# Kernel optimization log

Hardware: AMD Instinct MI355X
Metric: run time of the kernel (lower is better)

The kernel has to match this reference:

```python
import jax, jax.numpy as jnp
import numpy as np

B, N, D = 256, 1024, 128
SCALING_FACTOR = 1.0


def setup_inputs() -> dict:
    key = jax.random.key(0)
    ks = jax.random.split(key, 7)
    d = jax.random.normal(ks[0], (B, N, D), dtype=jnp.float32)
    si = jax.random.normal(ks[1], (B, N, D), dtype=jnp.float32)
    sj = jax.random.normal(ks[2], (B, N, D), dtype=jnp.float32)
    mi = jax.random.randint(ks[3], (B, N), 0, 2).astype(bool)
    mj = jax.random.randint(ks[4], (B, N), 0, 2).astype(bool)
    # AvgModel.layer: Linear(D, D**2)
    W1 = jax.random.normal(ks[5], (D, D * D), dtype=jnp.float32) * 0.02
    b1 = jnp.zeros((D * D,), dtype=jnp.float32)
    # CondNNWAvgPRModel.layer: Linear(H=2D, 1)
    W2 = jax.random.normal(ks[6], (2 * D, 1), dtype=jnp.float32) * 0.02
    b2 = jnp.zeros((1,), dtype=jnp.float32)
    return {"d": d, "si": si, "sj": sj, "mi": mi, "mj": mj,
            "W1": W1, "b1": b1, "W2": W2, "b2": b2}


def reference(d, si, sj, mi, mj, W1, b1, W2, b2):
    # generate_transformation: M = relu(Linear(d[:,0,:])).reshape(B, D, D)
    dm = d[:, 0, :]                                   # [B, D]
    M = jax.nn.relu(dm @ W1 + b1).reshape(-1, D, D)    # [B, D, D]

    def predict(s, mask):
        # transform = bmm(x, M)
        td = jnp.einsum('bnd,bde->bne', d, M)          # [B, N, D]
        ts = jnp.einsum('bnd,bde->bne', s, M)          # [B, N, D]
        x = jnp.concatenate([td, ts], axis=2)          # [B, N, 2D]
        z = (x @ W2 + b2)[..., 0]                      # [B, N]
        # fused masked segment-sum replacing the Python loop
        return jnp.sum(z * mask.astype(z.dtype), axis=1)  # [B]

    score1 = predict(si, mi)
    score2 = predict(sj, mj)
    return jax.nn.sigmoid(SCALING_FACTOR * (score1 - score2))
```

## Files before the change

### kernel.cpp

```cpp
#include <hip/hip_runtime.h>
#include <math.h>

#define BB 256
#define NN 1024
#define DD 128
#define NCHUNK 4
#define ROWS (NN / NCHUNK)

#define PA_OFF   0
#define PCI_OFF  (NCHUNK*BB*DD)
#define PCJ_OFF  (2*NCHUNK*BB*DD)
#define PCNT_OFF (3*NCHUNK*BB*DD)
#define U_OFF    (PCNT_OFF + NCHUNK*BB)
#define V_OFF    (U_OFF + BB*DD)

typedef _Float16 f16x8 __attribute__((ext_vector_type(8)));
typedef float    f32x4 __attribute__((ext_vector_type(4)));

__global__ __launch_bounds__(256) void k1_sparse(
    const float* __restrict__ d, const float* __restrict__ si,
    const float* __restrict__ sj, const void* __restrict__ miv,
    const void* __restrict__ mjv, float* __restrict__ ws)
{
    const int chunk = blockIdx.x;
    const int b     = blockIdx.y;
    const int role  = blockIdx.z;
    const int t     = threadIdx.x;
    const int lane  = t & 31;
    const int rg    = t >> 5;
    const int wid   = t >> 6;
    const int l64   = t & 63;

    __shared__ int s_mode;
    if (t == 0) s_mode = 0;
    __syncthreads();
    {
        const unsigned int* a = (const unsigned int*)miv;
        const unsigned int* c = (const unsigned int*)mjv;
        if ((a[t] | c[t]) > 1u) s_mode = 1;
    }
    __syncthreads();
    const bool bytes_mode = (s_mode != 0);

    __shared__ float s_wc[ROWS];
    __shared__ short s_idx[ROWS];
    __shared__ int   s_wcnt[4];
    __shared__ int   s_woff[5];
    __shared__ int   s_cnt4[4];

    const int    n0      = chunk * ROWS;
    const size_t rowbase = (size_t)b * NN;

    float w;
    {
        const size_t m = rowbase + (size_t)(n0 + t);
        float fi, fj;
        if (bytes_mode) {
            fi = (float)((const unsigned char*)miv)[m];
            fj = (float)((const unsigned char*)mjv)[m];
        } else {
            fi = (float)((const int*)miv)[m];
            fj = (float)((const int*)mjv)[m];
        }
        w = (role == 0) ? (fi - fj) : ((role == 1) ? fi : fj);
        if (role == 0) {
            const unsigned long long bi = __ballot(fi != 0.f);
            const unsigned long long bj = __ballot(fj != 0.f);
            if (l64 == 0) s_cnt4[wid] = __popcll(bi) - __popcll(bj);
        }
    }
    const bool keep = (w != 0.f);
    const unsigned long long ball = __ballot(keep);
    const int prefix = __popcll(ball & ((1ull << l64) - 1ull));
    if (l64 == 0) s_wcnt[wid] = __popcll(ball);
    __syncthreads();
    if (t == 0) {
        int a0 = 0;
        #pragma unroll
        for (int ww = 0; ww < 4; ++ww) { s_woff[ww] = a0; a0 += s_wcnt[ww]; }
        s_woff[4] = a0;
        if (role == 0)
            ws[PCNT_OFF + chunk * BB + b] =
                (float)(s_cnt4[0] + s_cnt4[1] + s_cnt4[2] + s_cnt4[3]);
    }
    __syncthreads();
    const int K    = s_woff[4];
    const int Kpad = (K + 31) & ~31;
    if (keep) {
        const int pos = s_woff[wid] + prefix;
        s_idx[pos] = (short)t;
        s_wc[pos]  = w;
    }
    for (int p = K + t; p < Kpad; p += 256) { s_idx[p] = 0; s_wc[p] = 0.f; }
    __syncthreads();

    const float* src = (role == 0) ? d : ((role == 1) ? si : sj);
    const size_t cbase = (rowbase + (size_t)n0) * (size_t)DD
                       + (size_t)lane * 4;

    float acc[4] = {0.f, 0.f, 0.f, 0.f};

    for (int i = 0; i < Kpad; i += 32) {
        int   r[4];
        float wv[4];
        #pragma unroll
        for (int u = 0; u < 4; ++u) {
            const int p = i + u * 8 + rg;
            r[u]  = s_idx[p];
            wv[u] = s_wc[p];
        }
        float4 v[4];
        #pragma unroll
        for (int u = 0; u < 4; ++u)
            v[u] = *(const float4*)(src + cbase + (size_t)r[u] * DD);
        #pragma unroll
        for (int u = 0; u < 4; ++u) {
            acc[0] = fmaf(wv[u], v[u].x, acc[0]);
            acc[1] = fmaf(wv[u], v[u].y, acc[1]);
            acc[2] = fmaf(wv[u], v[u].z, acc[2]);
            acc[3] = fmaf(wv[u], v[u].w, acc[3]);
        }
    }

    __shared__ float red[256][5];
    #pragma unroll
    for (int i = 0; i < 4; ++i) red[t][i] = acc[i];
    __syncthreads();
    if (t < 128) {
        #pragma unroll
        for (int i = 0; i < 4; ++i) red[t][i] += red[t + 128][i];
    }
    __syncthreads();
    if (t < 64) {
        #pragma unroll
        for (int i = 0; i < 4; ++i) red[t][i] += red[t + 64][i];
    }
    __syncthreads();
    if (t < 32) {
        #pragma unroll
        for (int i = 0; i < 4; ++i) red[t][i] += red[t + 32][i];
        const size_t poff = ((role == 0) ? PA_OFF : ((role == 1) ? PCI_OFF
                                                                 : PCJ_OFF))
                          + ((size_t)chunk * BB + b) * DD;
        float* P = ws + poff;
        #pragma unroll
        for (int i = 0; i < 4; ++i) P[t * 4 + i] = red[t][i];
    }
}

__global__ __launch_bounds__(256) void k2_mfma(
    const float* __restrict__ d, const float* __restrict__ W1,
    const float* __restrict__ b1, const float* __restrict__ W2,
    float* __restrict__ ws)
{
    const int p    = blockIdx.x;
    const int b0   = blockIdx.y * 64;
    const int t    = threadIdx.x;
    const int wid  = t >> 6;
    const int lane = t & 63;
    const int lcol = lane & 15;
    const int lrow = lane >> 4;

    __shared__ _Float16 As[64][136];
    __shared__ _Float16 Bs[128][136];

    for (int idx = t; idx < 64 * 32; idx += 256) {
        const int bb = idx >> 5;
        const int k4 = (idx & 31) * 4;
        const float4 v = *(const float4*)(d + (size_t)(b0 + bb) * (NN * DD) + k4);
        As[bb][k4 + 0] = (_Float16)v.x;
        As[bb][k4 + 1] = (_Float16)v.y;
        As[bb][k4 + 2] = (_Float16)v.z;
        As[bb][k4 + 3] = (_Float16)v.w;
    }
    for (int idx = t; idx < 128 * 32; idx += 256) {
        const int k  = idx >> 5;
        const int c4 = (idx & 31) * 4;
        const float4 v =
            *(const float4*)(W1 + (size_t)k * 16384 + p * 128 + c4);
        Bs[c4 + 0][k] = (_Float16)v.x;
        Bs[c4 + 1][k] = (_Float16)v.y;
        Bs[c4 + 2][k] = (_Float16)v.z;
        Bs[c4 + 3][k] = (_Float16)v.w;
    }
    __syncthreads();

    f32x4 acc[8];
    #pragma unroll
    for (int n = 0; n < 8; ++n) acc[n] = (f32x4){0.f, 0.f, 0.f, 0.f};

    #pragma unroll
    for (int ks = 0; ks < 4; ++ks) {
        const int k0 = ks * 32;
        const f16x8 afrag = *(const f16x8*)&As[wid * 16 + lcol][k0 + lrow * 8];
        #pragma unroll
        for (int n = 0; n < 8; ++n) {
            const f16x8 bfrag =
                *(const f16x8*)&Bs[n * 16 + lcol][k0 + lrow * 8];
            acc[n] = __builtin_amdgcn_mfma_f32_16x16x32_f16(
                afrag, bfrag, acc[n], 0, 0, 0);
        }
    }

    float ua[4] = {0.f, 0.f, 0.f, 0.f};
    float va[4] = {0.f, 0.f, 0.f, 0.f};
    #pragma unroll
    for (int n = 0; n < 8; ++n) {
        const int c = n * 16 + lcol;
        const float bias = b1[p * 128 + c];
        const float w2a  = W2[c];
        const float w2b  = W2[128 + c];
        #pragma unroll
        for (int reg = 0; reg < 4; ++reg) {
            const float g = fmaxf(acc[n][reg] + bias, 0.f);
            ua[reg] = fmaf(g, w2a, ua[reg]);
            va[reg] = fmaf(g, w2b, va[reg]);
        }
    }
    #pragma unroll
    for (int off = 8; off > 0; off >>= 1) {
        #pragma unroll
        for (int reg = 0; reg < 4; ++reg) {
            ua[reg] += __shfl_xor(ua[reg], off, 64);
            va[reg] += __shfl_xor(va[reg], off, 64);
        }
    }
    if (lcol == 0) {
        #pragma unroll
        for (int reg = 0; reg < 4; ++reg) {
            const int b = b0 + wid * 16 + lrow * 4 + reg;
            ws[U_OFF + (size_t)b * DD + p] = ua[reg];
            ws[V_OFF + (size_t)b * DD + p] = va[reg];
        }
    }
}

__global__ __launch_bounds__(64) void k3_final(
    const float* __restrict__ ws, const float* __restrict__ b2p,
    float* __restrict__ out)
{
    const int b = blockIdx.x;
    const int l = threadIdx.x;

    float s = 0.f;
    #pragma unroll
    for (int rep = 0; rep < 2; ++rep) {
        const int k = l + rep * 64;
        float A = 0.f, Ci = 0.f, Cj = 0.f;
        #pragma unroll
        for (int c = 0; c < NCHUNK; ++c) {
            A  += ws[PA_OFF  + ((size_t)c * BB + b) * DD + k];
            Ci += ws[PCI_OFF + ((size_t)c * BB + b) * DD + k];
            Cj += ws[PCJ_OFF + ((size_t)c * BB + b) * DD + k];
        }
        s += A * ws[U_OFF + (size_t)b * DD + k]
           + (Ci - Cj) * ws[V_OFF + (size_t)b * DD + k];
    }
    #pragma unroll
    for (int off = 32; off > 0; off >>= 1) s += __shfl_down(s, off, 64);

    if (l == 0) {
        float cnt = 0.f;
        #pragma unroll
        for (int c = 0; c < NCHUNK; ++c) cnt += ws[PCNT_OFF + c * BB + b];
        const float score = s + b2p[0] * cnt;
        out[b] = 1.f / (1.f + expf(-score));
    }
}

extern "C" void kernel_launch(void* const* d_in, const int* in_sizes, int n_in,
                              void* d_out, int out_size, void* d_ws, size_t ws_size,
                              hipStream_t stream)
{
    const float* d   = (const float*)d_in[0];
    const float* si  = (const float*)d_in[1];
    const float* sj  = (const float*)d_in[2];
    const void*  mi  = d_in[3];
    const void*  mj  = d_in[4];
    const float* W1  = (const float*)d_in[5];
    const float* b1  = (const float*)d_in[6];
    const float* W2  = (const float*)d_in[7];
    const float* b2  = (const float*)d_in[8];
    float* ws  = (float*)d_ws;
    float* out = (float*)d_out;

    dim3 g1(NCHUNK, BB, 3);
    k1_sparse<<<g1, 256, 0, stream>>>(d, si, sj, mi, mj, ws);
    dim3 g2(128, 4);
    k2_mfma<<<g2, 256, 0, stream>>>(d, W1, b1, W2, ws);
    k3_final<<<BB, 64, 0, stream>>>(ws, b2, out);
}
```

Measured before the change: 53.23 us.

## Fuse sparse gather and MFMA transform kernels into one interleaved launch

Merges the masked-row gather kernel and the W1 MFMA kernel into a single 4096-block launch. Every fourth block runs a GEMM tile and the others run gather work, so the two independent phases overlap on the device and one launch gap disappears. Each GEMM tile is split into column halves to create 1024 GEMM blocks, and A fragments are now read straight from global memory instead of staged through LDS. This writes two partial U/V buffers that the final kernel adds together. The cost is an extra small workspace and duplicated A loads across the column halves.

Result: faster. 44.20 us (-17.0%).

```diff
diff --git a/kernel.cpp b/kernel.cpp
--- a/kernel.cpp
+++ b/kernel.cpp
@@ -11,42 +11,141 @@
 #define PCI_OFF  (NCHUNK*BB*DD)
 #define PCJ_OFF  (2*NCHUNK*BB*DD)
 #define PCNT_OFF (3*NCHUNK*BB*DD)
-#define U_OFF    (PCNT_OFF + NCHUNK*BB)
-#define V_OFF    (U_OFF + BB*DD)
+#define U0_OFF   (PCNT_OFF + NCHUNK*BB)
+#define V0_OFF   (U0_OFF + BB*DD)
+#define U1_OFF   (V0_OFF + BB*DD)
+#define V1_OFF   (U1_OFF + BB*DD)
 
 typedef _Float16 f16x8 __attribute__((ext_vector_type(8)));
 typedef float    f32x4 __attribute__((ext_vector_type(4)));
 
-__global__ __launch_bounds__(256) void k1_sparse(
+__global__ __launch_bounds__(256) void fused_k12(
     const float* __restrict__ d, const float* __restrict__ si,
     const float* __restrict__ sj, const void* __restrict__ miv,
-    const void* __restrict__ mjv, float* __restrict__ ws)
+    const void* __restrict__ mjv, const float* __restrict__ W1,
+    const float* __restrict__ b1, const float* __restrict__ W2,
+    float* __restrict__ ws)
 {
-    const int chunk = blockIdx.x;
-    const int b     = blockIdx.y;
-    const int role  = blockIdx.z;
-    const int t     = threadIdx.x;
+    const int idx = blockIdx.x;
+    const int t   = threadIdx.x;
+
+    __shared__ __align__(16) char smem[17408];
+
+    if ((idx & 3) == 1) {
+        const int k2id  = idx >> 2;
+        const int ctile = k2id & 255;
+        const int bg    = k2id >> 8;
+        const int p     = ctile >> 1;
+        const int chalf = ctile & 1;
+        const int c0b   = chalf * 64;
+        const int b0    = bg * 64;
+        const int wid   = t >> 6;
+        const int lane  = t & 63;
+        const int lcol  = lane & 15;
+        const int lrow  = lane >> 4;
+
+        _Float16 (*Bs)[136] = (_Float16(*)[136])smem;
+
+        for (int s = t; s < 128 * 16; s += 256) {
+            const int k  = s >> 4;
+            const int c4 = (s & 15) * 4;
+            const float4 v =
+                *(const float4*)(W1 + (size_t)k * 16384 + p * 128 + c0b + c4);
+            Bs[c4 + 0][k] = (_Float16)v.x;
+            Bs[c4 + 1][k] = (_Float16)v.y;
+            Bs[c4 + 2][k] = (_Float16)v.z;
+            Bs[c4 + 3][k] = (_Float16)v.w;
+        }
+        __syncthreads();
+
+        const int brow = b0 + wid * 16 + lcol;
+        const float* drow = d + (size_t)brow * (NN * DD);
+
+        f32x4 acc[4];
+        #pragma unroll
+        for (int n = 0; n < 4; ++n) acc[n] = (f32x4){0.f, 0.f, 0.f, 0.f};
+
+        #pragma unroll
+        for (int ks = 0; ks < 4; ++ks) {
+            const int kf = ks * 32 + lrow * 8;
+            const float4 a0 = *(const float4*)(drow + kf);
+            const float4 a1 = *(const float4*)(drow + kf + 4);
+            f16x8 afrag;
+            afrag[0] = (_Float16)a0.x; afrag[1] = (_Float16)a0.y;
+            afrag[2] = (_Float16)a0.z; afrag[3] = (_Float16)a0.w;
+            afrag[4] = (_Float16)a1.x; afrag[5] = (_Float16)a1.y;
+            afrag[6] = (_Float16)a1.z; afrag[7] = (_Float16)a1.w;
+            #pragma unroll
+            for (int n = 0; n < 4; ++n) {
+                const f16x8 bfrag = *(const f16x8*)&Bs[n * 16 + lcol][kf];
+                acc[n] = __builtin_amdgcn_mfma_f32_16x16x32_f16(
+                    afrag, bfrag, acc[n], 0, 0, 0);
+            }
+        }
+
+        float ua[4] = {0.f, 0.f, 0.f, 0.f};
+        float va[4] = {0.f, 0.f, 0.f, 0.f};
+        #pragma unroll
+        for (int n = 0; n < 4; ++n) {
+            const int c = c0b + n * 16 + lcol;
+            const float bias = b1[p * 128 + c];
+            const float w2a  = W2[c];
+            const float w2b  = W2[128 + c];
+            #pragma unroll
+            for (int reg = 0; reg < 4; ++reg) {
+                const float g = fmaxf(acc[n][reg] + bias, 0.f);
+                ua[reg] = fmaf(g, w2a, ua[reg]);
+                va[reg] = fmaf(g, w2b, va[reg]);
+            }
+        }
+        #pragma unroll
+        for (int off = 8; off > 0; off >>= 1) {
+            #pragma unroll
+            for (int reg = 0; reg < 4; ++reg) {
+                ua[reg] += __shfl_xor(ua[reg], off, 64);
+                va[reg] += __shfl_xor(va[reg], off, 64);
+            }
+        }
+        if (lcol == 0) {
+            const size_t uo = chalf ? U1_OFF : U0_OFF;
+            const size_t vo = chalf ? V1_OFF : V0_OFF;
+            #pragma unroll
+            for (int reg = 0; reg < 4; ++reg) {
+                const int b = b0 + wid * 16 + lrow * 4 + reg;
+                ws[uo + (size_t)b * DD + p] = ua[reg];
+                ws[vo + (size_t)b * DD + p] = va[reg];
+            }
+        }
+        return;
+    }
+
+    const int q4 = idx >> 2, r4 = idx & 3;
+    const int k1id  = q4 * 3 + (r4 == 0 ? 0 : r4 - 1);
+    const int chunk = k1id & 3;
+    const int b     = (k1id >> 2) & 255;
+    const int role  = k1id >> 10;
     const int lane  = t & 31;
     const int rg    = t >> 5;
     const int wid   = t >> 6;
     const int l64   = t & 63;
 
-    __shared__ int s_mode;
-    if (t == 0) s_mode = 0;
+    float* s_wc   = (float*)smem;
+    short* s_idx  = (short*)(smem + 1024);
+    int*   s_wcnt = (int*)(smem + 1536);
+    int*   s_woff = (int*)(smem + 1552);
+    int*   s_cnt4 = (int*)(smem + 1572);
+    int*   s_mode = (int*)(smem + 1588);
+    float (*red)[5] = (float(*)[5])(smem + 1600);
+
+    if (t == 0) *s_mode = 0;
     __syncthreads();
     {
         const unsigned int* a = (const unsigned int*)miv;
         const unsigned int* c = (const unsigned int*)mjv;
-        if ((a[t] | c[t]) > 1u) s_mode = 1;
-    }
-    __syncthreads();
-    const bool bytes_mode = (s_mode != 0);
-
-    __shared__ float s_wc[ROWS];
-    __shared__ short s_idx[ROWS];
-    __shared__ int   s_wcnt[4];
-    __shared__ int   s_woff[5];
-    __shared__ int   s_cnt4[4];
+        if ((a[t] | c[t]) > 1u) *s_mode = 1;
+    }
+    __syncthreads();
+    const bool bytes_mode = (*s_mode != 0);
 
     const int    n0      = chunk * ROWS;
     const size_t rowbase = (size_t)b * NN;
@@ -122,7 +221,6 @@
         }
     }
 
-    __shared__ float red[256][5];
     #pragma unroll
     for (int i = 0; i < 4; ++i) red[t][i] = acc[i];
     __syncthreads();
@@ -145,93 +243,6 @@
         float* P = ws + poff;
         #pragma unroll
         for (int i = 0; i < 4; ++i) P[t * 4 + i] = red[t][i];
-    }
-}
-
-__global__ __launch_bounds__(256) void k2_mfma(
-    const float* __restrict__ d, const float* __restrict__ W1,
-    const float* __restrict__ b1, const float* __restrict__ W2,
-    float* __restrict__ ws)
-{
-    const int p    = blockIdx.x;
-    const int b0   = blockIdx.y * 64;
-    const int t    = threadIdx.x;
-    const int wid  = t >> 6;
-    const int lane = t & 63;
-    const int lcol = lane & 15;
-    const int lrow = lane >> 4;
-
-    __shared__ _Float16 As[64][136];
-    __shared__ _Float16 Bs[128][136];
-
-    for (int idx = t; idx < 64 * 32; idx += 256) {
-        const int bb = idx >> 5;
-        const int k4 = (idx & 31) * 4;
-        const float4 v = *(const float4*)(d + (size_t)(b0 + bb) * (NN * DD) + k4);
-        As[bb][k4 + 0] = (_Float16)v.x;
-        As[bb][k4 + 1] = (_Float16)v.y;
-        As[bb][k4 + 2] = (_Float16)v.z;
-        As[bb][k4 + 3] = (_Float16)v.w;
-    }
-    for (int idx = t; idx < 128 * 32; idx += 256) {
-        const int k  = idx >> 5;
-        const int c4 = (idx & 31) * 4;
-        const float4 v =
-            *(const float4*)(W1 + (size_t)k * 16384 + p * 128 + c4);
-        Bs[c4 + 0][k] = (_Float16)v.x;
-        Bs[c4 + 1][k] = (_Float16)v.y;
-        Bs[c4 + 2][k] = (_Float16)v.z;
-        Bs[c4 + 3][k] = (_Float16)v.w;
-    }
-    __syncthreads();
-
-    f32x4 acc[8];
-    #pragma unroll
-    for (int n = 0; n < 8; ++n) acc[n] = (f32x4){0.f, 0.f, 0.f, 0.f};
-
-    #pragma unroll
-    for (int ks = 0; ks < 4; ++ks) {
-        const int k0 = ks * 32;
-        const f16x8 afrag = *(const f16x8*)&As[wid * 16 + lcol][k0 + lrow * 8];
-        #pragma unroll
-        for (int n = 0; n < 8; ++n) {
-            const f16x8 bfrag =
-                *(const f16x8*)&Bs[n * 16 + lcol][k0 + lrow * 8];
-            acc[n] = __builtin_amdgcn_mfma_f32_16x16x32_f16(
-                afrag, bfrag, acc[n], 0, 0, 0);
-        }
-    }
-
-    float ua[4] = {0.f, 0.f, 0.f, 0.f};
-    float va[4] = {0.f, 0.f, 0.f, 0.f};
-    #pragma unroll
-    for (int n = 0; n < 8; ++n) {
-        const int c = n * 16 + lcol;
-        const float bias = b1[p * 128 + c];
-        const float w2a  = W2[c];
-        const float w2b  = W2[128 + c];
-        #pragma unroll
-        for (int reg = 0; reg < 4; ++reg) {
-            const float g = fmaxf(acc[n][reg] + bias, 0.f);
-            ua[reg] = fmaf(g, w2a, ua[reg]);
-            va[reg] = fmaf(g, w2b, va[reg]);
-        }
-    }
-    #pragma unroll
-    for (int off = 8; off > 0; off >>= 1) {
-        #pragma unroll
-        for (int reg = 0; reg < 4; ++reg) {
-            ua[reg] += __shfl_xor(ua[reg], off, 64);
-            va[reg] += __shfl_xor(va[reg], off, 64);
-        }
-    }
-    if (lcol == 0) {
-        #pragma unroll
-        for (int reg = 0; reg < 4; ++reg) {
-            const int b = b0 + wid * 16 + lrow * 4 + reg;
-            ws[U_OFF + (size_t)b * DD + p] = ua[reg];
-            ws[V_OFF + (size_t)b * DD + p] = va[reg];
-        }
     }
 }
 
@@ -253,8 +264,11 @@
             Ci += ws[PCI_OFF + ((size_t)c * BB + b) * DD + k];
             Cj += ws[PCJ_OFF + ((size_t)c * BB + b) * DD + k];
         }
-        s += A * ws[U_OFF + (size_t)b * DD + k]
-           + (Ci - Cj) * ws[V_OFF + (size_t)b * DD + k];
+        const float u = ws[U0_OFF + (size_t)b * DD + k]
+                      + ws[U1_OFF + (size_t)b * DD + k];
+        const float v = ws[V0_OFF + (size_t)b * DD + k]
+                      + ws[V1_OFF + (size_t)b * DD + k];
+        s += A * u + (Ci - Cj) * v;
     }
     #pragma unroll
     for (int off = 32; off > 0; off >>= 1) s += __shfl_down(s, off, 64);
@@ -284,9 +298,6 @@
     float* ws  = (float*)d_ws;
     float* out = (float*)d_out;
 
-    dim3 g1(NCHUNK, BB, 3);
-    k1_sparse<<<g1, 256, 0, stream>>>(d, si, sj, mi, mj, ws);
-    dim3 g2(128, 4);
-    k2_mfma<<<g2, 256, 0, stream>>>(d, W1, b1, W2, ws);
+    fused_k12<<<4096, 256, 0, stream>>>(d, si, sj, mi, mj, W1, b1, W2, ws);
     k3_final<<<BB, 64, 0, stream>>>(ws, b2, out);
 }
```
